# Performance work log

Hardware: AMD Instinct MI355X
Metric: run time of the kernel (lower is better)

## Reference

```python
import jax, jax.numpy as jnp
import numpy as np

N_NODES = 50000
N_EDGES = 800000
HIDDEN = 128
MSG = 128


def setup_inputs() -> dict:
    key = jax.random.key(0)
    ks = jax.random.split(key, 10)
    s = 0.05
    return {
        "x": jax.random.normal(ks[0], (N_NODES, HIDDEN), jnp.float32),
        "h": jax.random.normal(ks[1], (N_NODES, HIDDEN), jnp.float32),
        "src": jax.random.randint(ks[2], (N_EDGES,), 0, N_NODES, jnp.int32),
        "dst": jax.random.randint(ks[3], (N_EDGES,), 0, N_NODES, jnp.int32),
        "W_msg": s * jax.random.normal(ks[4], (MSG, 2 * HIDDEN), jnp.float32),
        "b_msg": s * jax.random.normal(ks[5], (MSG,), jnp.float32),
        "W_ih": s * jax.random.normal(ks[6], (3 * HIDDEN, HIDDEN + MSG), jnp.float32),
        "W_hh": s * jax.random.normal(ks[7], (3 * HIDDEN, HIDDEN), jnp.float32),
        "b_ih": s * jax.random.normal(ks[8], (3 * HIDDEN,), jnp.float32),
        "b_hh": s * jax.random.normal(ks[9], (3 * HIDDEN,), jnp.float32),
    }


def reference(x, h, src, dst, W_msg, b_msg, W_ih, W_hh, b_ih, b_hh):
    N = x.shape[0]
    # --- message: linear on concat(x_src, detached h_src) -> [E, MSG]
    h_det = jax.lax.stop_gradient(h)  # h.detach() in original
    feat = jnp.concatenate([x[src], h_det[src]], axis=1)  # [E, 2H]
    m = feat @ W_msg.T + b_msg  # [E, MSG]
    # --- mean aggregation over incoming edges; isolated nodes get zeros (DGL semantics)
    msum = jax.ops.segment_sum(m, dst, num_segments=N)  # [N, MSG]
    deg = jax.ops.segment_sum(jnp.ones((src.shape[0],), m.dtype), dst, num_segments=N)
    c = msum / jnp.maximum(deg, 1.0)[:, None]
    # --- GRUCell update (PyTorch GRUCell math)
    inp = jnp.concatenate([x, c], axis=1)  # [N, H+MSG]
    gi = inp @ W_ih.T + b_ih
    gh = h @ W_hh.T + b_hh
    i_r, i_z, i_n = jnp.split(gi, 3, axis=1)
    h_r, h_z, h_n = jnp.split(gh, 3, axis=1)
    r = jax.nn.sigmoid(i_r + h_r)
    z = jax.nn.sigmoid(i_z + h_z)
    n = jnp.tanh(i_n + r * h_n)
    return (1.0 - z) * n + z * h
```

## Files before the change

### kernel.cpp

```cpp
#include <hip/hip_runtime.h>

#define H 128
#define CAP 5120

typedef __attribute__((ext_vector_type(8))) short s16x8;
typedef __attribute__((ext_vector_type(2))) float f32x2;
typedef __attribute__((ext_vector_type(4))) float f32x4;

#define WAITBAR(N) asm volatile("s_waitcnt vmcnt(" #N ")\n\ts_barrier" ::: "memory")
#define BARO() asm volatile("s_barrier" ::: "memory")

__device__ __forceinline__ float bf2f(unsigned short u){
  unsigned x = ((unsigned)u) << 16;
  return __builtin_bit_cast(float, x);
}
__device__ __forceinline__ unsigned short f2bf(float f){
  unsigned u = __builtin_bit_cast(unsigned, f);
  u += 0x7fff + ((u >> 16) & 1);
  return (unsigned short)(u >> 16);
}

typedef __attribute__((address_space(1))) void gvoid;
typedef __attribute__((address_space(3))) void lvoid;
__device__ __forceinline__ void gload16(const void* g, void* l){
  __builtin_amdgcn_global_load_lds((gvoid*)(void*)g, (lvoid*)l, 16, 0, 0);
}

__global__ void pcfs_kernel(const float* x_, const float* h, const int* src, const int* dst,
                            const float* W_msg, const float* W_ih, const float* W_hh,
                            const float* b_ih, const float* b_hh,
                            unsigned short* xhs, unsigned char* xq,
                            unsigned* bucketArr, int* bucketCnt,
                            unsigned short* WmsgT, unsigned short* WbigT, float* biasb,
                            int NB, int YE, int nv, int E){
  int blk = blockIdx.x, tid = threadIdx.x;
  if(blk < YE){
    __shared__ int hcnt[256];
    __shared__ int hpos[256];
    hcnt[tid] = 0;
    __syncthreads();
    int base = blk*2048;
    unsigned pk[8]; int bk[8];
    #pragma unroll
    for(int it=0; it<8; ++it){
      int e = base + it*256 + tid;
      bk[it] = -1;
      if(e < E){
        int d = dst[e], s = src[e];
        pk[it] = ((unsigned)d << 16) | (unsigned)s;
        int b = d >> 8;
        bk[it] = b;
        atomicAdd(&hcnt[b], 1);
      }
    }
    __syncthreads();
    if(tid < NB){
      int c = hcnt[tid];
      hpos[tid] = (c > 0) ? atomicAdd(&bucketCnt[tid*32], c) : 0;
    }
    __syncthreads();
    #pragma unroll
    for(int it=0; it<8; ++it){
      if(bk[it] >= 0){
        int p = atomicAdd(&hpos[bk[it]], 1);
        if(p < CAP) bucketArr[(long)bk[it]*CAP + p] = pk[it];
      }
    }
    return;
  }
  long w0 = (long)(blk - YE)*2048 + tid;
  const int NW = 512*384;
  #pragma unroll 1
  for(int it=0; it<8; ++it){
    long w = w0 + (long)it*256;
    if(w < 2L*nv){
      const float* sp; long j; int add;
      if(w < nv){ sp = x_; j = w; add = 0; }
      else { sp = h; j = w - nv; add = 128; }
      float4 v = ((const float4*)sp)[j];
      ushort4 o; o.x=f2bf(v.x); o.y=f2bf(v.y); o.z=f2bf(v.z); o.w=f2bf(v.w);
      int node = (int)(j >> 5), col = add + ((int)j & 31)*4;
      int k = col >> 5, wc = col & 31;
      *(ushort4*)(xhs + (long)k*nv + node*32 + wc) = o;
      int r = __builtin_amdgcn_cvt_pk_fp8_f32(v.x, v.y, 0, false);
      r = __builtin_amdgcn_cvt_pk_fp8_f32(v.z, v.w, r, true);
      *(unsigned int*)(xq + (long)k*nv + node*32 + wc) = (unsigned)r;
      continue;
    }
    long i = w - 2L*nv;
    if(i < NW){
      int hf = (int)(i / 98304); int r1 = (int)(i % 98304);
      int kt = r1 / 16384; int r2 = r1 % 16384;
      int row = r2 / 64;   int r3 = r2 % 64;
      int cw = r3 >> 3;    int j = r3 & 7;
      int c = cw ^ (row & 7);
      int k = kt*64 + c*8 + j;
      int rp = hf*256 + row;
      int q = rp >> 2, g = rp & 3;
      float v;
      if(g < 3){
        int orow = g*128 + q;
        v = (k < 256) ? W_ih[orow*256 + k] : W_hh[orow*128 + (k-256)];
      } else {
        v = (k < 256) ? 0.f : W_hh[(256 + q)*128 + (k-256)];
      }
      WbigT[i] = f2bf(v);
    } else if(i < NW + 128*256){
      int j2 = (int)(i - NW);
      int kt = j2 / 8192; int r2 = j2 % 8192;
      int row = r2 / 64;  int r3 = r2 % 64;
      int cw = r3 >> 3;   int j = r3 & 7;
      int c = cw ^ (row & 7);
      int k = kt*64 + c*8 + j;
      WmsgT[j2] = f2bf(W_msg[row*256 + k]);
    } else if(i < NW + 128*256 + 512){
      int r = (int)(i - NW - 128*256);
      int q = r >> 2, g = r & 3;
      biasb[r] = (g < 3) ? (b_ih[g*128+q] + b_hh[g*128+q]) : b_hh[256+q];
    }
  }
}

__global__ void fill2_kernel(const unsigned* bucketArr, const int* bucketCnt,
                             int* rc, unsigned short* ss16, int N){
  __shared__ int lcnt[256];
  int b = blockIdx.x, tid = threadIdx.x;
  lcnt[tid] = 0;
  __syncthreads();
  int cnt = bucketCnt[b*32]; if(cnt > CAP) cnt = CAP;
  int nbase = b << 8;
  const unsigned* arr = bucketArr + (long)b*CAP;
  for(int i = tid; i < cnt; i += 256){
    unsigned e = arr[i];
    int d = e >> 16, s = e & 0xffff;
    int p = atomicAdd(&lcnt[d - nbase], 1);
    if(p < 128) ss16[((long)d << 7) + p] = (unsigned short)s;
  }
  __syncthreads();
  int node = nbase + tid;
  if(node < N) rc[node] = lcnt[tid];
}

__global__ __launch_bounds__(256, 8) void agg_kernel(
    const unsigned char* xq, const int* rc, const unsigned short* ss16,
    unsigned short* Sb, int N){
  int tid = threadIdx.x;
  int group = tid >> 2, sub = tid & 3;
  int node = blockIdx.y*64 + group;
  if(node >= N) return;
  const unsigned char* base = xq + (long)blockIdx.x*(long)N*32;
  int cnt = rc[node];
  int use = (cnt < 128) ? cnt : 128;
  const long e0 = (long)node << 7;
  int co = sub*8;
  float a[8] = {0.f,0.f,0.f,0.f,0.f,0.f,0.f,0.f};
  #define ACC8(q) { \
    f32x2 l0 = __builtin_amdgcn_cvt_pk_f32_fp8((q).x, false); \
    f32x2 h0 = __builtin_amdgcn_cvt_pk_f32_fp8((q).x, true);  \
    f32x2 l1 = __builtin_amdgcn_cvt_pk_f32_fp8((q).y, false); \
    f32x2 h1 = __builtin_amdgcn_cvt_pk_f32_fp8((q).y, true);  \
    a[0]+=l0[0]; a[1]+=l0[1]; a[2]+=h0[0]; a[3]+=h0[1]; \
    a[4]+=l1[0]; a[5]+=l1[1]; a[6]+=h1[0]; a[7]+=h1[1]; }
  int i = 0;
  for(; i+7 < use; i += 8){
    ushort4 ia = *(const ushort4*)(ss16 + e0 + i);
    ushort4 ib = *(const ushort4*)(ss16 + e0 + i + 4);
    uint2 q0 = *(const uint2*)(base + (long)ia.x*32 + co);
    uint2 q1 = *(const uint2*)(base + (long)ia.y*32 + co);
    uint2 q2 = *(const uint2*)(base + (long)ia.z*32 + co);
    uint2 q3 = *(const uint2*)(base + (long)ia.w*32 + co);
    uint2 q4 = *(const uint2*)(base + (long)ib.x*32 + co);
    uint2 q5 = *(const uint2*)(base + (long)ib.y*32 + co);
    uint2 q6 = *(const uint2*)(base + (long)ib.z*32 + co);
    uint2 q7 = *(const uint2*)(base + (long)ib.w*32 + co);
    ACC8(q0); ACC8(q1); ACC8(q2); ACC8(q3);
    ACC8(q4); ACC8(q5); ACC8(q6); ACC8(q7);
  }
  for(; i+3 < use; i += 4){
    ushort4 ia = *(const ushort4*)(ss16 + e0 + i);
    uint2 q0 = *(const uint2*)(base + (long)ia.x*32 + co);
    uint2 q1 = *(const uint2*)(base + (long)ia.y*32 + co);
    uint2 q2 = *(const uint2*)(base + (long)ia.z*32 + co);
    uint2 q3 = *(const uint2*)(base + (long)ia.w*32 + co);
    ACC8(q0); ACC8(q1); ACC8(q2); ACC8(q3);
  }
  for(; i < use; ++i){
    int s0 = ss16[e0 + i];
    uint2 q0 = *(const uint2*)(base + (long)s0*32 + co);
    ACC8(q0);
  }
  #undef ACC8
  float inv = (cnt > 0) ? 1.0f/(float)cnt : 0.f;
  unsigned short o[8];
  #pragma unroll
  for(int j=0;j<8;++j) o[j] = f2bf(a[j]*inv);
  *(s16x8*)(Sb + (long)node*256 + blockIdx.x*32 + co) = *(const s16x8*)o;
}

__global__ __launch_bounds__(512, 2) void fused_kernel(
    const unsigned short* xhs, const unsigned short* Sb,
    const unsigned short* WmsgT, const unsigned short* WbigT,
    const float* b_msg, const float* biasb, const int* deg,
    float* outp, int NN){
  __shared__ __align__(16) char lds[131072];
  char* W0 = lds;
  char* W1 = lds + 32768;
  char* N0 = lds + 65536;
  char* N1 = lds + 81920;
  char* ldsC = lds + 98304;
  float* ldsO = (float*)(lds + 32768);

  int tid = threadIdx.x;
  int lane = tid & 63, wv = tid >> 6;
  int l15 = lane & 15, l4 = lane >> 4;
  long nodebase = (long)blockIdx.x * 128;
  const long NV = (long)NN * 32;
  const f32x4 fz = {0.f,0.f,0.f,0.f};

  auto stageS = [&](int koff, char* dst){
    #pragma unroll
    for(int it=0; it<2; ++it){
      int slot = it*512 + tid;
      int row = slot >> 3, cw = slot & 7;
      int c = cw ^ (row & 7);
      long gr = nodebase + row; if(gr > NN-1) gr = NN-1;
      gload16(Sb + gr*256 + koff + c*8, dst + it*8192 + wv*1024);
    }
  };
  auto stageX = [&](int koff, char* dst){
    #pragma unroll
    for(int it=0; it<2; ++it){
      int slot = it*512 + tid;
      int row = slot >> 3, cw = slot & 7;
      int c = cw ^ (row & 7);
      int col = koff + c*8;
      int k = col >> 5, wc = col & 31;
      long gr = nodebase + row; if(gr > NN-1) gr = NN-1;
      gload16(xhs + (long)k*NV + gr*32 + wc, dst + it*8192 + wv*1024);
    }
  };
  auto stageW1k = [&](int kt, char* dst){
    #pragma unroll
    for(int it=0; it<2; ++it){
      int slot = it*512 + tid;
      gload16(WmsgT + kt*8192 + slot*8, dst + it*8192 + wv*1024);
    }
  };
  auto stageW3k = [&](int idx, char* dst){
    #pragma unroll
    for(int it=0; it<4; ++it){
      int slot = it*512 + tid;
      gload16(WbigT + (long)idx*16384 + slot*8, dst + it*8192 + wv*1024);
    }
  };

  int wm1 = wv >> 2, wn1 = wv & 3;
  f32x4 acc1[4][2];
  #pragma unroll
  for(int m=0;m<4;++m){ acc1[m][0]=fz; acc1[m][1]=fz; }

  auto compute1 = [&](const char* Wb, const char* Nb){
    __builtin_amdgcn_s_setprio(1);
    #pragma unroll
    for(int kk=0; kk<2; ++kk){
      s16x8 af[4], bn[2];
      #pragma unroll
      for(int m=0;m<4;++m){
        int fr = wm1*64 + m*16 + l15;
        af[m] = *(const s16x8*)(Wb + fr*128 + (((kk*4+l4) ^ (fr&7))*16));
      }
      #pragma unroll
      for(int n=0;n<2;++n){
        int nr = wn1*32 + n*16 + l15;
        bn[n] = *(const s16x8*)(Nb + nr*128 + (((kk*4+l4) ^ (nr&7))*16));
      }
      #pragma unroll
      for(int m=0;m<4;++m)
        #pragma unroll
        for(int n=0;n<2;++n)
          acc1[m][n] = __builtin_amdgcn_mfma_f32_16x16x32_bf16(af[m], bn[n], acc1[m][n], 0, 0, 0);
    }
    __builtin_amdgcn_s_setprio(0);
  };

  stageW1k(0, W0); stageS(0, N0);
  stageW1k(1, W1); stageS(64, N1);
  WAITBAR(4); compute1(W0, N0); BARO();
  stageW1k(2, W0); stageS(128, N0);
  WAITBAR(4); compute1(W1, N1); BARO();
  stageW1k(3, W1); stageS(192, N1);
  WAITBAR(4); compute1(W0, N0); BARO();
  stageW3k(0, W0); stageX(0, N0);
  WAITBAR(6); compute1(W1, N1); BARO();

  #pragma unroll
  for(int n=0;n<2;++n){
    int node_l = wn1*32 + n*16 + l15;
    long gn = nodebase + node_l; if(gn > NN-1) gn = NN-1;
    int dg = deg[gn];
    float msk = (dg > 0) ? 1.f : 0.f;
    #pragma unroll
    for(int m=0;m<4;++m){
      int ccb = wm1*64 + m*16 + l4*4;
      float4 bm = *(const float4*)(b_msg + ccb);
      ushort4 o;
      o.x = f2bf((acc1[m][n][0] + bm.x)*msk);
      o.y = f2bf((acc1[m][n][1] + bm.y)*msk);
      o.z = f2bf((acc1[m][n][2] + bm.z)*msk);
      o.w = f2bf((acc1[m][n][3] + bm.w)*msk);
      *(ushort4*)(ldsC + node_l*256 + (((ccb>>3) ^ (node_l&7))*16) + (ccb&4)*2) = o;
    }
  }
  __syncthreads();

  int wm = wv >> 1, wn = wv & 1;

  auto runHalf = [&](int hf){
    f32x4 acc3[4][4];
    #pragma unroll
    for(int m=0;m<4;++m)
      #pragma unroll
      for(int n=0;n<4;++n) acc3[m][n] = fz;

    auto computeN = [&](const char* Wb, const char* Nb){
      __builtin_amdgcn_s_setprio(1);
      #pragma unroll
      for(int kk=0; kk<2; ++kk){
        s16x8 af[4], bn[4];
        #pragma unroll
        for(int m=0;m<4;++m){
          int fr = wm*64 + m*16 + l15;
          af[m] = *(const s16x8*)(Wb + fr*128 + (((kk*4+l4) ^ (fr&7))*16));
        }
        #pragma unroll
        for(int n=0;n<4;++n){
          int nr = wn*64 + n*16 + l15;
          bn[n] = *(const s16x8*)(Nb + nr*128 + (((kk*4+l4) ^ (nr&7))*16));
        }
        #pragma unroll
        for(int m=0;m<4;++m)
          #pragma unroll
          for(int n=0;n<4;++n)
            acc3[m][n] = __builtin_amdgcn_mfma_f32_16x16x32_bf16(af[m], bn[n], acc3[m][n], 0, 0, 0);
      }
      __builtin_amdgcn_s_setprio(0);
    };
    auto computeC = [&](const char* Wb, int ktc){
      __builtin_amdgcn_s_setprio(1);
      #pragma unroll
      for(int kk=0; kk<2; ++kk){
        s16x8 af[4], bn[4];
        #pragma unroll
        for(int m=0;m<4;++m){
          int fr = wm*64 + m*16 + l15;
          af[m] = *(const s16x8*)(Wb + fr*128 + (((kk*4+l4) ^ (fr&7))*16));
        }
        #pragma unroll
        for(int n=0;n<4;++n){
          int nr = wn*64 + n*16 + l15;
          bn[n] = *(const s16x8*)(ldsC + nr*256 + (((ktc*8 + kk*4 + l4) ^ (nr&7))*16));
        }
        #pragma unroll
        for(int m=0;m<4;++m)
          #pragma unroll
          for(int n=0;n<4;++n)
            acc3[m][n] = __builtin_amdgcn_mfma_f32_16x16x32_bf16(af[m], bn[n], acc3[m][n], 0, 0, 0);
      }
      __builtin_amdgcn_s_setprio(0);
    };

    if(hf == 1) stageX(0, N0);
    stageW3k(hf*6+1, W1); stageX(64, N1);
    WAITBAR(6); computeN(W0, N0); BARO();
    stageW3k(hf*6+2, W0);
    WAITBAR(4); computeN(W1, N1); BARO();
    stageW3k(hf*6+3, W1);
    WAITBAR(4); computeC(W0, 0); BARO();
    stageW3k(hf*6+4, W0); stageX(128, N0);
    WAITBAR(6); computeC(W1, 1); BARO();
    stageW3k(hf*6+5, W1); stageX(192, N1);
    WAITBAR(6); computeN(W0, N0); BARO();
    if(hf == 0){
      stageW3k(6, W0);
      WAITBAR(4); computeN(W1, N1); BARO();
    } else {
      WAITBAR(0); computeN(W1, N1); BARO();
    }

    const char* hbuf = (hf == 0) ? N0 : N1;
    #pragma unroll
    for(int m=0;m<4;++m){
      int q = hf*64 + wm*16 + m*4 + l4;
      int ql = q & 63;
      float4 bb = *(const float4*)(biasb + q*4);
      #pragma unroll
      for(int n=0;n<4;++n){
        int node_l = wn*64 + n*16 + l15;
        unsigned short hu = *(const unsigned short*)(hbuf + node_l*128 +
                              (((ql>>3) ^ (node_l&7))*16) + (ql&7)*2);
        float hv = bf2f(hu);
        float vr  = acc3[m][n][0] + bb.x;
        float vz  = acc3[m][n][1] + bb.y;
        float vsn = acc3[m][n][2] + bb.z;
        float vhn = acc3[m][n][3] + bb.w;
        float r = 1.f/(1.f + __expf(-vr));
        float z = 1.f/(1.f + __expf(-vz));
        float narg = vsn + (r - 1.f)*vhn;
        float nn2 = 2.f/(1.f + __expf(-2.f*narg)) - 1.f;
        ldsO[node_l*64 + (ql ^ ((node_l & 15) << 2))] = (1.f - z)*nn2 + z*hv;
      }
    }
    __syncthreads();

    #pragma unroll
    for(int it=0; it<4; ++it){
      int slot = it*512 + tid;
      int node_l = slot >> 4, f4 = slot & 15;
      long gn = nodebase + node_l;
      if(gn < NN){
        float4 v = *(const float4*)(ldsO + node_l*64 + (((f4*4) ^ ((node_l & 15) << 2))));
        *(float4*)(outp + gn*128 + hf*64 + f4*4) = v;
      }
    }
    __syncthreads();
  };

  runHalf(0);
  runHalf(1);
}

extern "C" void kernel_launch(void* const* d_in, const int* in_sizes, int n_in,
                              void* d_out, int out_size, void* d_ws, size_t ws_size,
                              hipStream_t stream){
  const float* x     = (const float*)d_in[0];
  const float* h     = (const float*)d_in[1];
  const int*   src   = (const int*)d_in[2];
  const int*   dst   = (const int*)d_in[3];
  const float* W_msg = (const float*)d_in[4];
  const float* b_msg = (const float*)d_in[5];
  const float* W_ih  = (const float*)d_in[6];
  const float* W_hh  = (const float*)d_in[7];
  const float* b_ih  = (const float*)d_in[8];
  const float* b_hh  = (const float*)d_in[9];
  const int N = in_sizes[0] / H;
  const int E = in_sizes[2];
  float* out = (float*)d_out;

  char* p = (char*)d_ws;
  auto alloc = [&](size_t bytes)->char*{
    char* r = p; p += (bytes + 255) & ~(size_t)255; return r;
  };
  unsigned short* xhs   = (unsigned short*)alloc((size_t)N*256*2);
  unsigned short* Sb    = (unsigned short*)alloc((size_t)N*256*2);
  unsigned char*  xq    = (unsigned char*)alloc((size_t)N*256);
  unsigned short* WmsgT = (unsigned short*)alloc(128*256*2);
  unsigned short* WbigT = (unsigned short*)alloc(512*384*2);
  float*          biasb = (float*)alloc(512*4);
  int*            rc    = (int*)alloc((size_t)N*4);
  unsigned short* ss16  = (unsigned short*)alloc((size_t)N*128*2);
  int NB = (N + 255) >> 8;
  unsigned*       bktA  = (unsigned*)alloc((size_t)NB*CAP*4);
  int*            bktC  = (int*)alloc((size_t)NB*32*4);

  hipMemsetAsync(bktC, 0, (size_t)NB*32*4, stream);
  int nv = N*H/4;
  const int NPREP = 512*384 + 128*256 + 512;
  int YE = (E + 2047)/2048;
  long convTotal = 2L*nv + NPREP;
  int YC = (int)((convTotal + 2047)/2048);
  pcfs_kernel<<<YE + YC, 256, 0, stream>>>(
      x, h, src, dst, W_msg, W_ih, W_hh, b_ih, b_hh,
      xhs, xq, bktA, bktC, WmsgT, WbigT, biasb, NB, YE, nv, E);

  fill2_kernel<<<NB, 256, 0, stream>>>(bktA, bktC, rc, ss16, N);

  dim3 gagg(8, (N + 63)/64);
  agg_kernel<<<gagg, 256, 0, stream>>>(xq, rc, ss16, Sb, N);

  int nblk = (N + 127)/128;
  fused_kernel<<<nblk, 512, 0, stream>>>(
      xhs, Sb, WmsgT, WbigT, b_msg, biasb, rc, out, N);
}
```

Baseline: 128.9 us.

## Shrink fused kernel LDS to single-buffer and spill message result to global

Cuts the fused GEMM kernel's shared memory from 128KB to 48KB by dropping double buffering and keeping the intermediate message matrix C in a global scratch buffer instead of LDS. Launch bounds rise to 6 waves per SIMD so more blocks can be resident and hide latency through occupancy rather than software pipelining. Output is written straight from registers, with no LDS transpose. The cost is a full wait and barrier on every k-step, extra global traffic for C, and uncoalesced scalar stores of the output.

```diff
diff --git a/kernel.cpp b/kernel.cpp
--- a/kernel.cpp
+++ b/kernel.cpp
@@ -197,18 +197,14 @@
   *(s16x8*)(Sb + (long)node*256 + blockIdx.x*32 + co) = *(const s16x8*)o;
 }
 
-__global__ __launch_bounds__(512, 2) void fused_kernel(
-    const unsigned short* xhs, const unsigned short* Sb,
+__global__ __launch_bounds__(512, 6) void fused_kernel(
+    const unsigned short* xhs, const unsigned short* Sb, unsigned short* cb,
     const unsigned short* WmsgT, const unsigned short* WbigT,
     const float* b_msg, const float* biasb, const int* deg,
     float* outp, int NN){
-  __shared__ __align__(16) char lds[131072];
-  char* W0 = lds;
-  char* W1 = lds + 32768;
-  char* N0 = lds + 65536;
-  char* N1 = lds + 81920;
-  char* ldsC = lds + 98304;
-  float* ldsO = (float*)(lds + 32768);
+  __shared__ __align__(16) char lds[49152];
+  char* Wb = lds;
+  char* Nb = lds + 32768;
 
   int tid = threadIdx.x;
   int lane = tid & 63, wv = tid >> 6;
@@ -217,17 +213,31 @@
   const long NV = (long)NN * 32;
   const f32x4 fz = {0.f,0.f,0.f,0.f};
 
-  auto stageS = [&](int koff, char* dst){
+  auto stageW1k = [&](int kt){
+    #pragma unroll
+    for(int it=0; it<2; ++it){
+      int slot = it*512 + tid;
+      gload16(WmsgT + kt*8192 + slot*8, Wb + it*8192 + wv*1024);
+    }
+  };
+  auto stageW3k = [&](int idx){
+    #pragma unroll
+    for(int it=0; it<4; ++it){
+      int slot = it*512 + tid;
+      gload16(WbigT + (long)idx*16384 + slot*8, Wb + it*8192 + wv*1024);
+    }
+  };
+  auto stageS = [&](int koff){
     #pragma unroll
     for(int it=0; it<2; ++it){
       int slot = it*512 + tid;
       int row = slot >> 3, cw = slot & 7;
       int c = cw ^ (row & 7);
       long gr = nodebase + row; if(gr > NN-1) gr = NN-1;
-      gload16(Sb + gr*256 + koff + c*8, dst + it*8192 + wv*1024);
-    }
-  };
-  auto stageX = [&](int koff, char* dst){
+      gload16(Sb + gr*256 + koff + c*8, Nb + it*8192 + wv*1024);
+    }
+  };
+  auto stageX = [&](int koff){
     #pragma unroll
     for(int it=0; it<2; ++it){
       int slot = it*512 + tid;
@@ -236,22 +246,23 @@
       int col = koff + c*8;
       int k = col >> 5, wc = col & 31;
       long gr = nodebase + row; if(gr > NN-1) gr = NN-1;
-      gload16(xhs + (long)k*NV + gr*32 + wc, dst + it*8192 + wv*1024);
-    }
-  };
-  auto stageW1k = [&](int kt, char* dst){
+      gload16(xhs + (long)k*NV + gr*32 + wc, Nb + it*8192 + wv*1024);
+    }
+  };
+  auto stageC = [&](int koff){
     #pragma unroll
     for(int it=0; it<2; ++it){
       int slot = it*512 + tid;
-      gload16(WmsgT + kt*8192 + slot*8, dst + it*8192 + wv*1024);
-    }
-  };
-  auto stageW3k = [&](int idx, char* dst){
-    #pragma unroll
-    for(int it=0; it<4; ++it){
-      int slot = it*512 + tid;
-      gload16(WbigT + (long)idx*16384 + slot*8, dst + it*8192 + wv*1024);
-    }
+      int row = slot >> 3, cw = slot & 7;
+      int c = cw ^ (row & 7);
+      long gr = nodebase + row; if(gr > NN-1) gr = NN-1;
+      gload16(cb + gr*128 + koff + c*8, Nb + it*8192 + wv*1024);
+    }
+  };
+  auto stageK = [&](int kidx){
+    if(kidx < 2) stageX(kidx*64);
+    else if(kidx < 4) stageC((kidx-2)*64);
+    else stageX(128 + (kidx-4)*64);
   };
 
   int wm1 = wv >> 2, wn1 = wv & 3;
@@ -259,7 +270,10 @@
   #pragma unroll
   for(int m=0;m<4;++m){ acc1[m][0]=fz; acc1[m][1]=fz; }
 
-  auto compute1 = [&](const char* Wb, const char* Nb){
+  #pragma unroll
+  for(int kt=0; kt<4; ++kt){
+    stageW1k(kt); stageS(kt*64);
+    WAITBAR(0);
     __builtin_amdgcn_s_setprio(1);
     #pragma unroll
     for(int kk=0; kk<2; ++kk){
@@ -281,48 +295,48 @@
           acc1[m][n] = __builtin_amdgcn_mfma_f32_16x16x32_bf16(af[m], bn[n], acc1[m][n], 0, 0, 0);
     }
     __builtin_amdgcn_s_setprio(0);
-  };
-
-  stageW1k(0, W0); stageS(0, N0);
-  stageW1k(1, W1); stageS(64, N1);
-  WAITBAR(4); compute1(W0, N0); BARO();
-  stageW1k(2, W0); stageS(128, N0);
-  WAITBAR(4); compute1(W1, N1); BARO();
-  stageW1k(3, W1); stageS(192, N1);
-  WAITBAR(4); compute1(W0, N0); BARO();
-  stageW3k(0, W0); stageX(0, N0);
-  WAITBAR(6); compute1(W1, N1); BARO();
-
+    BARO();
+  }
+  {
+    float msk1[2];
+    #pragma unroll
+    for(int n=0;n<2;++n){
+      long gn = nodebase + wn1*32 + n*16 + l15; if(gn > NN-1) gn = NN-1;
+      msk1[n] = (deg[gn] > 0) ? 1.f : 0.f;
+    }
+    #pragma unroll
+    for(int m=0;m<4;++m){
+      int cc0 = wm1*64 + m*16 + l4*4;
+      float4 bm = *(const float4*)(b_msg + cc0);
+      #pragma unroll
+      for(int n=0;n<2;++n){
+        long gn = nodebase + wn1*32 + n*16 + l15;
+        if(gn < NN){
+          ushort4 o;
+          o.x = f2bf((acc1[m][n][0] + bm.x)*msk1[n]);
+          o.y = f2bf((acc1[m][n][1] + bm.y)*msk1[n]);
+          o.z = f2bf((acc1[m][n][2] + bm.z)*msk1[n]);
+          o.w = f2bf((acc1[m][n][3] + bm.w)*msk1[n]);
+          *(ushort4*)(cb + gn*128 + cc0) = o;
+        }
+      }
+    }
+  }
+
+  int wm = wv >> 1, wn = wv & 1;
   #pragma unroll
-  for(int n=0;n<2;++n){
-    int node_l = wn1*32 + n*16 + l15;
-    long gn = nodebase + node_l; if(gn > NN-1) gn = NN-1;
-    int dg = deg[gn];
-    float msk = (dg > 0) ? 1.f : 0.f;
-    #pragma unroll
-    for(int m=0;m<4;++m){
-      int ccb = wm1*64 + m*16 + l4*4;
-      float4 bm = *(const float4*)(b_msg + ccb);
-      ushort4 o;
-      o.x = f2bf((acc1[m][n][0] + bm.x)*msk);
-      o.y = f2bf((acc1[m][n][1] + bm.y)*msk);
-      o.z = f2bf((acc1[m][n][2] + bm.z)*msk);
-      o.w = f2bf((acc1[m][n][3] + bm.w)*msk);
-      *(ushort4*)(ldsC + node_l*256 + (((ccb>>3) ^ (node_l&7))*16) + (ccb&4)*2) = o;
-    }
-  }
-  __syncthreads();
-
-  int wm = wv >> 1, wn = wv & 1;
-
-  auto runHalf = [&](int hf){
+  for(int hf=0; hf<2; ++hf){
     f32x4 acc3[4][4];
     #pragma unroll
     for(int m=0;m<4;++m)
       #pragma unroll
       for(int n=0;n<4;++n) acc3[m][n] = fz;
 
-    auto computeN = [&](const char* Wb, const char* Nb){
+    #pragma unroll
+    for(int kt=0; kt<6; ++kt){
+      int kk2 = (kt < 4) ? kt : ((kt == 4) ? (hf==0 ? 5 : 4) : (hf==0 ? 4 : 5));
+      stageW3k(hf*6 + kk2); stageK(kk2);
+      WAITBAR(0);
       __builtin_amdgcn_s_setprio(1);
       #pragma unroll
       for(int kk=0; kk<2; ++kk){
@@ -344,61 +358,31 @@
             acc3[m][n] = __builtin_amdgcn_mfma_f32_16x16x32_bf16(af[m], bn[n], acc3[m][n], 0, 0, 0);
       }
       __builtin_amdgcn_s_setprio(0);
-    };
-    auto computeC = [&](const char* Wb, int ktc){
-      __builtin_amdgcn_s_setprio(1);
-      #pragma unroll
-      for(int kk=0; kk<2; ++kk){
-        s16x8 af[4], bn[4];
-        #pragma unroll
-        for(int m=0;m<4;++m){
-          int fr = wm*64 + m*16 + l15;
-          af[m] = *(const s16x8*)(Wb + fr*128 + (((kk*4+l4) ^ (fr&7))*16));
-        }
-        #pragma unroll
-        for(int n=0;n<4;++n){
-          int nr = wn*64 + n*16 + l15;
-          bn[n] = *(const s16x8*)(ldsC + nr*256 + (((ktc*8 + kk*4 + l4) ^ (nr&7))*16));
-        }
-        #pragma unroll
-        for(int m=0;m<4;++m)
-          #pragma unroll
-          for(int n=0;n<4;++n)
-            acc3[m][n] = __builtin_amdgcn_mfma_f32_16x16x32_bf16(af[m], bn[n], acc3[m][n], 0, 0, 0);
-      }
-      __builtin_amdgcn_s_setprio(0);
-    };
-
-    if(hf == 1) stageX(0, N0);
-    stageW3k(hf*6+1, W1); stageX(64, N1);
-    WAITBAR(6); computeN(W0, N0); BARO();
-    stageW3k(hf*6+2, W0);
-    WAITBAR(4); computeN(W1, N1); BARO();
-    stageW3k(hf*6+3, W1);
-    WAITBAR(4); computeC(W0, 0); BARO();
-    stageW3k(hf*6+4, W0); stageX(128, N0);
-    WAITBAR(6); computeC(W1, 1); BARO();
-    stageW3k(hf*6+5, W1); stageX(192, N1);
-    WAITBAR(6); computeN(W0, N0); BARO();
-    if(hf == 0){
-      stageW3k(6, W0);
-      WAITBAR(4); computeN(W1, N1); BARO();
-    } else {
-      WAITBAR(0); computeN(W1, N1); BARO();
-    }
-
-    const char* hbuf = (hf == 0) ? N0 : N1;
+      BARO();
+    }
+
+    float hv[4][4];
     #pragma unroll
     for(int m=0;m<4;++m){
       int q = hf*64 + wm*16 + m*4 + l4;
-      int ql = q & 63;
-      float4 bb = *(const float4*)(biasb + q*4);
+      int hq = q & 63;
       #pragma unroll
       for(int n=0;n<4;++n){
         int node_l = wn*64 + n*16 + l15;
-        unsigned short hu = *(const unsigned short*)(hbuf + node_l*128 +
-                              (((ql>>3) ^ (node_l&7))*16) + (ql&7)*2);
-        float hv = bf2f(hu);
+        unsigned short hu = *(const unsigned short*)(Nb + node_l*128 +
+                              (((hq>>3) ^ (node_l&7))*16) + (hq&7)*2);
+        hv[m][n] = bf2f(hu);
+      }
+    }
+    __syncthreads();
+
+    #pragma unroll
+    for(int m=0;m<4;++m){
+      int q = hf*64 + wm*16 + m*4 + l4;
+      float4 bb = *(const float4*)(biasb + q*4);
+      #pragma unroll
+      for(int n=0;n<4;++n){
+        long gn = nodebase + wn*64 + n*16 + l15;
         float vr  = acc3[m][n][0] + bb.x;
         float vz  = acc3[m][n][1] + bb.y;
         float vsn = acc3[m][n][2] + bb.z;
@@ -407,26 +391,10 @@
         float z = 1.f/(1.f + __expf(-vz));
         float narg = vsn + (r - 1.f)*vhn;
         float nn2 = 2.f/(1.f + __expf(-2.f*narg)) - 1.f;
-        ldsO[node_l*64 + (ql ^ ((node_l & 15) << 2))] = (1.f - z)*nn2 + z*hv;
-      }
-    }
-    __syncthreads();
-
-    #pragma unroll
-    for(int it=0; it<4; ++it){
-      int slot = it*512 + tid;
-      int node_l = slot >> 4, f4 = slot & 15;
-      long gn = nodebase + node_l;
-      if(gn < NN){
-        float4 v = *(const float4*)(ldsO + node_l*64 + (((f4*4) ^ ((node_l & 15) << 2))));
-        *(float4*)(outp + gn*128 + hf*64 + f4*4) = v;
-      }
-    }
-    __syncthreads();
-  };
-
-  runHalf(0);
-  runHalf(1);
+        if(gn < NN) outp[gn*128 + q] = (1.f - z)*nn2 + z*hv[m][n];
+      }
+    }
+  }
 }
 
 extern "C" void kernel_launch(void* const* d_in, const int* in_sizes, int n_in,
@@ -453,6 +421,7 @@
   unsigned short* xhs   = (unsigned short*)alloc((size_t)N*256*2);
   unsigned short* Sb    = (unsigned short*)alloc((size_t)N*256*2);
   unsigned char*  xq    = (unsigned char*)alloc((size_t)N*256);
+  unsigned short* cb    = (unsigned short*)alloc((size_t)N*128*2);
   unsigned short* WmsgT = (unsigned short*)alloc(128*256*2);
   unsigned short* WbigT = (unsigned short*)alloc(512*384*2);
   float*          biasb = (float*)alloc(512*4);
@@ -479,5 +448,5 @@
 
   int nblk = (N + 127)/128;
   fused_kernel<<<nblk, 512, 0, stream>>>(
-      xhs, Sb, WmsgT, WbigT, b_msg, biasb, rc, out, N);
-}
+      xhs, Sb, cb, WmsgT, WbigT, b_msg, biasb, rc, out, N);
+}
```

Result: slower. 261.7 us (+103.0%).
